# Kernel tuning notes

Hardware: AMD Instinct MI355X
Metric: run time of the kernel (lower is better)

The kernel has to match this reference:

```python
import jax, jax.numpy as jnp
import numpy as np

B = 32768          # number of graphs
NN = 19            # nodes per graph
N = B * NN         # total nodes
EF_PER, ES_PER = 120, 60
NUM_BANDS = 5
EPS = 1e-5


def _make_edges(e_per, seed):
    r = np.random.default_rng(seed)
    s = r.integers(0, NN, e_per)
    d = r.integers(0, NN, e_per)
    off = (np.arange(B, dtype=np.int64) * NN)[:, None]
    src = (off + s[None, :]).reshape(-1).astype(np.int32)
    dst = (off + d[None, :]).reshape(-1).astype(np.int32)
    return np.stack([src, dst], axis=0)  # [2, B*e_per]


def setup_inputs() -> dict:
    key = jax.random.key(0)
    ks = jax.random.split(key, 16)
    inp = {
        "x": jax.random.normal(ks[0], (N, NUM_BANDS), jnp.float32),
        "edge_weight_func": jax.random.uniform(ks[1], (B * EF_PER,), jnp.float32),
        "edge_index_func": jnp.asarray(_make_edges(EF_PER, 1)),
        "edge_index_struct": jnp.asarray(_make_edges(ES_PER, 2)),
        # GCN band params
        "W1": jax.random.normal(ks[2], (NUM_BANDS, 1, 32), jnp.float32) * 0.5,
        "b1": jnp.zeros((NUM_BANDS, 32), jnp.float32),
        "g1": jnp.ones((NUM_BANDS, 32), jnp.float32),
        "bt1": jnp.zeros((NUM_BANDS, 32), jnp.float32),
        "W2": jax.random.normal(ks[3], (NUM_BANDS, 32, 2), jnp.float32) * 0.2,
        "b2": jnp.zeros((NUM_BANDS, 2), jnp.float32),
        "g2": jnp.ones((NUM_BANDS, 2), jnp.float32),
        "bt2": jnp.zeros((NUM_BANDS, 2), jnp.float32),
        # MLP head (kaiming-ish fan_in init)
        "lin1_W": jax.random.normal(ks[4], (190, 128), jnp.float32) * np.sqrt(2.0 / 190),
        "lin1_b": jnp.zeros((128,), jnp.float32),
        "g3": jnp.ones((128,), jnp.float32),
        "bt3": jnp.zeros((128,), jnp.float32),
        "lin2_W": jax.random.normal(ks[5], (128, 32), jnp.float32) * np.sqrt(2.0 / 128),
        "lin2_b": jnp.zeros((32,), jnp.float32),
        "lin3_W": jax.random.normal(ks[6], (32, 2), jnp.float32) * np.sqrt(2.0 / 32),
        "lin3_b": jnp.zeros((2,), jnp.float32),
    }
    return inp


def _bn(h, g, b):
    # BatchNorm1d with batch statistics (training-mode math, deterministic)
    m = h.mean(0)
    v = h.var(0)
    return (h - m) * jax.lax.rsqrt(v + EPS) * g + b


def _gcn(h_in, W, b, src, dst, ew, n):
    # PyG GCNConv: symmetric norm with self-loops (fill 1), linear then scatter-add
    h = h_in @ W                                   # [N, out]
    deg = jax.ops.segment_sum(ew, dst, num_segments=n) + 1.0  # self-loop weight 1
    dinv = jax.lax.rsqrt(deg)
    norm = dinv[src] * ew * dinv[dst]              # [E]
    agg = jax.ops.segment_sum(norm[:, None] * h[src], dst, num_segments=n)
    return agg + (dinv * dinv)[:, None] * h + b    # self-loop term + bias


def reference(x, edge_weight_func, W1, b1, g1, bt1, W2, b2, g2, bt2,
              lin1_W, lin1_b, g3, bt3, lin2_W, lin2_b, lin3_W, lin3_b,
              edge_index_func, edge_index_struct):
    n = x.shape[0]
    bsz = n // NN
    sf, df = edge_index_func[0], edge_index_func[1]
    ss, ds = edge_index_struct[0], edge_index_struct[1]
    ew_s = jnp.ones((ss.shape[0],), x.dtype)
    outs = []
    for i in range(NUM_BANDS):
        h = _gcn(x[:, i:i + 1], W1[i], b1[i], sf, df, edge_weight_func, n)
        h = jax.nn.relu(_bn(h, g1[i], bt1[i]))
        h = _gcn(h, W2[i], b2[i], ss, ds, ew_s, n)
        h = jax.nn.relu(_bn(h, g2[i], bt2[i]))
        outs.append(h.reshape(bsz, NN * 2))
    xc = jnp.concatenate(outs, axis=1)             # [B, 190]
    h = jax.nn.relu(_bn(xc @ lin1_W + lin1_b, g3, bt3))
    h = jax.nn.relu(h @ lin2_W + lin2_b)
    return h @ lin3_W + lin3_b                     # [B, 2]
```

## Files before the change

kernel.cpp:

```cpp
#include <hip/hip_runtime.h>
#include <hip/hip_fp16.h>

#define BGR 32768
#define NNODE 19
#define NTOT (BGR*NNODE)
#define EF 120
#define ES 60
#define NB 5
#define EPS 1e-5f

#define WS_U     0
#define WS_PRE2  (WS_U + NTOT*NB)
#define WS_PRE3  (WS_PRE2 + BGR*190)
#define WS_H2    (WS_PRE3 + BGR*128)
#define WS_P3    (WS_H2 + NTOT*NB)
#define WS_R3    (WS_P3 + 2048*256)
#define WS_R1    (WS_R3 + 64*256)
#define WS_R2    (WS_R1 + 320)
#define WS_T1    (WS_R2 + 6400)
#define WS_A2    (WS_T1 + 660)
#define WS_D2    (WS_A2 + 16)
#define WS_A3    (WS_D2 + 16)
#define WS_D3    (WS_A3 + 128)

__global__ __launch_bounds__(256) void k1_gcn1(
    const float* __restrict__ x, const float* __restrict__ ew,
    const int* __restrict__ srcf, const int* __restrict__ dstf,
    float* __restrict__ Ub)
{
    __shared__ float xg[4][96];
    __shared__ float Nr[4][380];
    __shared__ float dinv[4][20];
    int t = threadIdx.x, q = t >> 6, lane = t & 63;
    int g = blockIdx.x*4 + q;

    int s0, d0, s1 = 0, d1 = 0; float w0, w1 = 0.f;
    bool e1 = (lane < EF - 64);
    s0 = srcf[g*EF+lane] - g*NNODE; d0 = dstf[g*EF+lane] - g*NNODE; w0 = ew[g*EF+lane];
    if (e1) { s1 = srcf[g*EF+lane+64] - g*NNODE; d1 = dstf[g*EF+lane+64] - g*NNODE; w1 = ew[g*EF+lane+64]; }
    for (int i = lane; i < 95; i += 64) xg[q][i] = x[g*95 + i];
    for (int i = lane; i < 380; i += 64) Nr[q][i] = 0.f;
    __syncthreads();

    atomicAdd(&Nr[q][d0*20 + s0], w0);
    if (e1) atomicAdd(&Nr[q][d1*20 + s1], w1);
    __syncthreads();

    if (lane < NNODE) {
        float s = 0.f;
        #pragma unroll
        for (int k = 0; k < 19; k++) s += Nr[q][lane*20 + k];
        dinv[q][lane] = rsqrtf(s + 1.f);
    }
    __syncthreads();
    for (int i = lane; i < 95; i += 64) xg[q][i] *= dinv[q][i/5];
    __syncthreads();

    for (int i = lane; i < 95; i += 64) {
        int b = i/19, v = i - 19*b;
        float acc = xg[q][v*5 + b];
        #pragma unroll
        for (int s = 0; s < 19; s++) acc += Nr[q][v*20 + s] * xg[q][s*5 + b];
        Ub[(size_t)b*NTOT + g*19 + v] = dinv[q][v] * acc;
    }
}

__global__ __launch_bounds__(256) void kr1(const float* __restrict__ U, float* __restrict__ r1)
{
    const float4* base = (const float4*)(U + (size_t)blockIdx.x * (NTOT/32));
    float s = 0.f, qq = 0.f;
    for (int n = (int)threadIdx.x; n < NTOT/128; n += 256) {
        float4 v = base[n];
        s += v.x + v.y + v.z + v.w;
        qq += v.x*v.x + v.y*v.y + v.z*v.z + v.w*v.w;
    }
    __shared__ float red[256][2];
    red[threadIdx.x][0] = s; red[threadIdx.x][1] = qq;
    __syncthreads();
    for (int off = 128; off > 0; off >>= 1) {
        if ((int)threadIdx.x < off) {
            red[threadIdx.x][0] += red[threadIdx.x+off][0];
            red[threadIdx.x][1] += red[threadIdx.x+off][1];
        }
        __syncthreads();
    }
    if (threadIdx.x < 2) r1[blockIdx.x*2 + threadIdx.x] = red[0][threadIdx.x];
}

__global__ __launch_bounds__(256) void k2b(const float* __restrict__ r1,
    const float* __restrict__ W1, const float* __restrict__ g1, const float* __restrict__ bt1,
    const float* __restrict__ W2, float4* __restrict__ T1)
{
    __shared__ float mean[5], varr[5];
    int t = threadIdx.x;
    if (t < 5) {
        float s = 0.f, qq = 0.f;
        for (int j = 0; j < 32; j++) { s += r1[(t*32+j)*2]; qq += r1[(t*32+j)*2+1]; }
        float m = s / (float)NTOT;
        mean[t] = m;
        varr[t] = qq / (float)NTOT - m*m;
    }
    __syncthreads();
    if (t < 160) {
        int b = t >> 5;
        float w = W1[t];
        float c = w * rsqrtf(w*w*varr[b] + EPS) * g1[t];
        T1[b*33 + (t & 31)] = make_float4(c, bt1[t] - c*mean[b], W2[t*2], W2[t*2+1]);
    }
}

__global__ __launch_bounds__(256) void k3a(
    const float* __restrict__ Ub, const float4* __restrict__ T1p,
    unsigned int* __restrict__ H2)
{
    int bb = blockIdx.x / (NTOT/256);
    int node = (blockIdx.x - bb*(NTOT/256))*256 + (int)threadIdx.x;
    float uv = Ub[(size_t)bb*NTOT + node];
    const float4* Tb = T1p + bb*33;
    float hx = 0.f, hy = 0.f;
    #pragma unroll
    for (int f = 0; f < 32; f++) {
        float4 c = Tb[f];
        float r = fmaxf(fmaf(c.x, uv, c.y), 0.f);
        hx = fmaf(r, c.z, hx);
        hy = fmaf(r, c.w, hy);
    }
    __half2 h = __floats2half2_rn(hx, hy);
    H2[(size_t)bb*NTOT + node] = *(unsigned int*)&h;
}

__global__ __launch_bounds__(256) void k3b(
    const unsigned int* __restrict__ H2, const int* __restrict__ srcs, const int* __restrict__ dsts,
    const float* __restrict__ b2, float2* __restrict__ pre2)
{
    __shared__ float2 h2l[4][96];
    __shared__ float  Mr[4][380];
    __shared__ float  dinv[4][20];
    __shared__ float  b2l[12];
    int t = threadIdx.x, q = t >> 6, lane = t & 63;
    int g = blockIdx.x*4 + q;

    int b0 = lane/19, v0 = lane - 19*b0;
    unsigned int h0 = H2[(size_t)b0*NTOT + g*19 + v0];
    int b1 = (lane+64)/19, v1 = (lane+64) - 19*b1;
    unsigned int h1 = (lane < 31) ? H2[(size_t)b1*NTOT + g*19 + v1] : 0u;
    int ls = 0, ld = 0; bool ee = (lane < ES);
    if (ee) { ls = srcs[g*ES+lane] - g*NNODE; ld = dsts[g*ES+lane] - g*NNODE; }
    if (t < 10) b2l[t] = b2[t];
    for (int i = lane; i < 380; i += 64) Mr[q][i] = 0.f;
    __syncthreads();

    if (ee) atomicAdd(&Mr[q][ld*20 + ls], 1.f);
    __syncthreads();

    if (lane < NNODE) {
        float s = 0.f;
        #pragma unroll
        for (int k = 0; k < 19; k++) s += Mr[q][lane*20 + k];
        dinv[q][lane] = rsqrtf(s + 1.f);
    }
    __syncthreads();

    {
        float2 f0 = __half22float2(*(__half2*)&h0);
        float sc = dinv[q][v0];
        h2l[q][v0*5 + b0] = make_float2(f0.x*sc, f0.y*sc);
        if (lane < 31) {
            float2 f1 = __half22float2(*(__half2*)&h1);
            float sc1 = dinv[q][v1];
            h2l[q][v1*5 + b1] = make_float2(f1.x*sc1, f1.y*sc1);
        }
    }
    __syncthreads();

    for (int i = lane; i < 95; i += 64) {
        int v = i/5, b = i - 5*v;
        float2 acc = h2l[q][i];
        #pragma unroll
        for (int s = 0; s < 19; s++) {
            float m = Mr[q][v*20 + s];
            float2 hh = h2l[q][s*5 + b];
            acc.x = fmaf(m, hh.x, acc.x);
            acc.y = fmaf(m, hh.y, acc.y);
        }
        float dv = dinv[q][v];
        pre2[(size_t)g*95 + i] = make_float2(fmaf(dv, acc.x, b2l[2*b]),
                                             fmaf(dv, acc.y, b2l[2*b+1]));
    }
}

__global__ __launch_bounds__(256) void kr2(const float2* __restrict__ pre2, float* __restrict__ r2)
{
    int t = threadIdx.x;
    size_t base = (size_t)blockIdx.x * 9728;
    float sx[5], sy[5], qx[5], qy[5];
    #pragma unroll
    for (int b = 0; b < 5; b++) { sx[b]=0.f; sy[b]=0.f; qx[b]=0.f; qy[b]=0.f; }
    for (int n = 0; n < 38; n++) {
        size_t i = base + n*256 + t;
        float2 v = pre2[i];
        int p = (int)(i % 95);
        int b = p % 5;
        #pragma unroll
        for (int bb = 0; bb < 5; bb++) {
            bool m = (b == bb);
            sx[bb] += m ? v.x : 0.f;     sy[bb] += m ? v.y : 0.f;
            qx[bb] += m ? v.x*v.x : 0.f; qy[bb] += m ? v.y*v.y : 0.f;
        }
    }
    __shared__ float red[256][20];
    #pragma unroll
    for (int b = 0; b < 5; b++) {
        red[t][2*b] = sx[b];      red[t][2*b+1] = sy[b];
        red[t][10+2*b] = qx[b];   red[t][11+2*b] = qy[b];
    }
    __syncthreads();
    for (int off = 128; off > 0; off >>= 1) {
        if (t < off) {
            #pragma unroll
            for (int k = 0; k < 20; k++) red[t][k] += red[t+off][k];
        }
        __syncthreads();
    }
    if (t < 20) r2[blockIdx.x*20 + t] = red[0][t];
}

__global__ __launch_bounds__(320) void k4b(const float* __restrict__ r2,
    const float* __restrict__ g2, const float* __restrict__ bt2,
    float* __restrict__ A2, float* __restrict__ D2)
{
    __shared__ float part[16][20];
    int t = threadIdx.x;
    int col = t % 20, grp = t / 20;
    float s = 0.f;
    for (int j = 0; j < 20; j++) s += r2[(grp*20 + j)*20 + col];
    part[grp][col] = s;
    __syncthreads();
    if (t < 20) {
        float ss = 0.f;
        #pragma unroll
        for (int j = 0; j < 16; j++) ss += part[j][t];
        part[0][t] = ss;
    }
    __syncthreads();
    if (t < 10) {
        float m = part[0][t] / (float)NTOT;
        float v = part[0][10+t] / (float)NTOT - m*m;
        float a = g2[t] * rsqrtf(v + EPS);
        A2[t] = a;
        D2[t] = bt2[t] - a*m;
    }
}

__global__ __launch_bounds__(256) void k5_lin1(
    const float2* __restrict__ pre2, const float* __restrict__ A2, const float* __restrict__ D2,
    const float* __restrict__ W, const float* __restrict__ bias,
    float* __restrict__ pre3, float* __restrict__ p3)
{
    __shared__ float xg[32*192];
    __shared__ float a2l[10], d2l[10];
    __shared__ float redS[4][128], redQ[4][128];
    int t = threadIdx.x, bid = blockIdx.x;
    if (t < 10) { a2l[t] = A2[t]; d2l[t] = D2[t]; }
    if (t < 64) xg[(t>>1)*192 + 190 + (t&1)] = 0.f;
    __syncthreads();

    const float2* src = pre2 + (size_t)bid*3040;
    for (int i = t; i < 3040; i += 256) {
        int gg = i / 95, p = i - gg*95;
        int b = p % 5;
        float2 v = src[i];
        xg[gg*192 + 2*p]     = fmaxf(fmaf(a2l[2*b],   v.x, d2l[2*b]),   0.f);
        xg[gg*192 + 2*p + 1] = fmaxf(fmaf(a2l[2*b+1], v.y, d2l[2*b+1]), 0.f);
    }
    __syncthreads();

    int f = t & 63, h = t >> 6;
    const float* xh = xg + h*8*192;
    float accA[8], accB[8];
    #pragma unroll
    for (int r = 0; r < 8; r++) { accA[r] = 0.f; accB[r] = 0.f; }

    for (int kt = 0; kt < 12; kt++) {
        float wA[16], wB[16];
        #pragma unroll
        for (int j = 0; j < 16; j++) {
            int k = kt*16 + j;
            if (k < 190) {
                int p = k >> 1, kk = k & 1;
                int v = p/5, b = p - 5*v;
                int row = b*38 + v*2 + kk;
                wA[j] = W[row*128 + f];
                wB[j] = W[row*128 + f + 64];
            } else { wA[j] = 0.f; wB[j] = 0.f; }
        }
        #pragma unroll
        for (int r = 0; r < 8; r++) {
            const float4* xr = (const float4*)(xh + r*192 + kt*16);
            #pragma unroll
            for (int jj = 0; jj < 4; jj++) {
                float4 xv = xr[jj];
                accA[r] = fmaf(xv.x, wA[4*jj+0], accA[r]);
                accA[r] = fmaf(xv.y, wA[4*jj+1], accA[r]);
                accA[r] = fmaf(xv.z, wA[4*jj+2], accA[r]);
                accA[r] = fmaf(xv.w, wA[4*jj+3], accA[r]);
                accB[r] = fmaf(xv.x, wB[4*jj+0], accB[r]);
                accB[r] = fmaf(xv.y, wB[4*jj+1], accB[r]);
                accB[r] = fmaf(xv.z, wB[4*jj+2], accB[r]);
                accB[r] = fmaf(xv.w, wB[4*jj+3], accB[r]);
            }
        }
    }

    float bb0 = bias[f], bb1 = bias[f + 64];
    float sA = 0.f, qA = 0.f, sB = 0.f, qB = 0.f;
    int g0 = bid*32 + h*8;
    #pragma unroll
    for (int r = 0; r < 8; r++) {
        float pA = accA[r] + bb0;
        float pB = accB[r] + bb1;
        pre3[(size_t)(g0+r)*128 + f]      = pA;
        pre3[(size_t)(g0+r)*128 + f + 64] = pB;
        sA += pA; qA += pA*pA;
        sB += pB; qB += pB*pB;
    }
    redS[h][f] = sA; redS[h][f+64] = sB;
    redQ[h][f] = qA; redQ[h][f+64] = qB;
    __syncthreads();
    if (t < 128) {
        p3[bid*256 + t] = redS[0][t] + redS[1][t] + redS[2][t] + redS[3][t];
    } else {
        int f2 = t - 128;
        p3[bid*256 + 128 + f2] = redQ[0][f2] + redQ[1][f2] + redQ[2][f2] + redQ[3][f2];
    }
}

__global__ __launch_bounds__(256) void k6a(const float* __restrict__ p3, float* __restrict__ r3)
{
    int j = blockIdx.x, f = threadIdx.x;
    float s = 0.f;
    for (int r = j*16; r < (j+1)*16; r++) s += p3[r*256 + f];
    r3[j*256 + f] = s;
}

__global__ __launch_bounds__(128) void k6b(const float* __restrict__ r3,
    const float* __restrict__ g3, const float* __restrict__ bt3,
    float* __restrict__ A3, float* __restrict__ D3)
{
    int f = threadIdx.x;
    float s = 0.f, q = 0.f;
    for (int j = 0; j < 64; j++) { s += r3[j*256 + f]; q += r3[j*256 + 128 + f]; }
    float m = s / (float)BGR;
    float v = q / (float)BGR - m*m;
    float a = g3[f] * rsqrtf(v + EPS);
    A3[f] = a;
    D3[f] = bt3[f] - a*m;
}

__global__ __launch_bounds__(256) void k7_head(
    const float* __restrict__ pre3, const float* __restrict__ A3, const float* __restrict__ D3,
    const float* __restrict__ W2h, const float* __restrict__ b2h,
    const float* __restrict__ W3h, const float* __restrict__ b3h,
    float* __restrict__ out)
{
    int g = blockIdx.x*256 + threadIdx.x;
    float accj[32];
    #pragma unroll
    for (int j = 0; j < 32; j++) accj[j] = b2h[j];
    const float* p3 = pre3 + (size_t)g*128;
    #pragma unroll 2
    for (int f4 = 0; f4 < 128; f4 += 4) {
        float4 pv = *(const float4*)(p3 + f4);
        float y0 = fmaxf(fmaf(A3[f4+0], pv.x, D3[f4+0]), 0.f);
        float y1 = fmaxf(fmaf(A3[f4+1], pv.y, D3[f4+1]), 0.f);
        float y2 = fmaxf(fmaf(A3[f4+2], pv.z, D3[f4+2]), 0.f);
        float y3 = fmaxf(fmaf(A3[f4+3], pv.w, D3[f4+3]), 0.f);
        #pragma unroll
        for (int j = 0; j < 32; j++) {
            accj[j] = fmaf(y0, W2h[(f4+0)*32+j], accj[j]);
            accj[j] = fmaf(y1, W2h[(f4+1)*32+j], accj[j]);
            accj[j] = fmaf(y2, W2h[(f4+2)*32+j], accj[j]);
            accj[j] = fmaf(y3, W2h[(f4+3)*32+j], accj[j]);
        }
    }
    float o0 = b3h[0], o1 = b3h[1];
    #pragma unroll
    for (int j = 0; j < 32; j++) {
        float yj = fmaxf(accj[j], 0.f);
        o0 = fmaf(yj, W3h[j*2+0], o0);
        o1 = fmaf(yj, W3h[j*2+1], o1);
    }
    ((float2*)out)[g] = make_float2(o0, o1);
}

extern "C" void kernel_launch(void* const* d_in, const int* in_sizes, int n_in,
                              void* d_out, int out_size, void* d_ws, size_t ws_size,
                              hipStream_t stream)
{
    (void)in_sizes; (void)n_in; (void)out_size; (void)ws_size;
    const float* x    = (const float*)d_in[0];
    const float* ew   = (const float*)d_in[1];
    const int*   eif  = (const int*)d_in[2];
    const int*   eis  = (const int*)d_in[3];
    const float* W1   = (const float*)d_in[4];
    const float* g1   = (const float*)d_in[6];
    const float* bt1  = (const float*)d_in[7];
    const float* W2   = (const float*)d_in[8];
    const float* b2   = (const float*)d_in[9];
    const float* g2   = (const float*)d_in[10];
    const float* bt2  = (const float*)d_in[11];
    const float* l1W  = (const float*)d_in[12];
    const float* l1b  = (const float*)d_in[13];
    const float* g3   = (const float*)d_in[14];
    const float* bt3  = (const float*)d_in[15];
    const float* l2W  = (const float*)d_in[16];
    const float* l2b  = (const float*)d_in[17];
    const float* l3W  = (const float*)d_in[18];
    const float* l3b  = (const float*)d_in[19];
    float* out = (float*)d_out;
    float* ws  = (float*)d_ws;

    const int* srcf = eif;  const int* dstf = eif + BGR*EF;
    const int* srcs = eis;  const int* dsts = eis + BGR*ES;

    float* U    = ws + WS_U;
    float* PRE2 = ws + WS_PRE2;
    float* PRE3 = ws + WS_PRE3;
    unsigned int* H2 = (unsigned int*)(ws + WS_H2);
    float* P3   = ws + WS_P3;
    float* R3   = ws + WS_R3;
    float* R1   = ws + WS_R1;
    float* R2   = ws + WS_R2;
    float4* T1  = (float4*)(ws + WS_T1);
    float* A2   = ws + WS_A2;
    float* D2   = ws + WS_D2;
    float* A3   = ws + WS_A3;
    float* D3   = ws + WS_D3;

    k1_gcn1<<<BGR/4, 256, 0, stream>>>(x, ew, srcf, dstf, U);
    kr1<<<160, 256, 0, stream>>>(U, R1);
    k2b<<<1, 256, 0, stream>>>(R1, W1, g1, bt1, W2, T1);
    k3a<<<(NTOT/256)*5, 256, 0, stream>>>(U, T1, H2);
    k3b<<<BGR/4, 256, 0, stream>>>(H2, srcs, dsts, b2, (float2*)PRE2);
    kr2<<<320, 256, 0, stream>>>((const float2*)PRE2, R2);
    k4b<<<1, 320, 0, stream>>>(R2, g2, bt2, A2, D2);
    k5_lin1<<<1024, 256, 0, stream>>>((const float2*)PRE2, A2, D2, l1W, l1b, PRE3, P3);
    k6a<<<64, 256, 0, stream>>>(P3, R3);
    k6b<<<1, 128, 0, stream>>>(R3, g3, bt3, A3, D3);
    k7_head<<<BGR/256, 256, 0, stream>>>(PRE3, A3, D3, l2W, l2b, l3W, l3b, out);
}
```

Measured before the change: 322.6 us.

## Fuse BN statistic partials into GCN kernels and prepermute lin1 weights

The GCN1 and GCN2 kernels now emit per-block sum and sum-of-squares partials through shared-memory atomics, which removes the separate kr1 and kr2 passes that re-read U and PRE2 from global memory. The single-block finalize kernels now reduce 8192 partials each using 1024 threads. A new kwp kernel writes the lin1 weight matrix in a permuted, zero-padded layout, so k5_lin1 drops its per-element index arithmetic and uses a 4x4 register tile. The shared matrices are padded to 20 columns so the inner loops can use float4 reads. The trade-off is serial final reductions over many partials in one block and an extra small weight-permutation launch on every call.

```diff
diff --git a/kernel.cpp b/kernel.cpp
--- a/kernel.cpp
+++ b/kernel.cpp
@@ -14,10 +14,11 @@
 #define WS_PRE3  (WS_PRE2 + BGR*190)
 #define WS_H2    (WS_PRE3 + BGR*128)
 #define WS_P3    (WS_H2 + NTOT*NB)
-#define WS_R3    (WS_P3 + 2048*256)
-#define WS_R1    (WS_R3 + 64*256)
-#define WS_R2    (WS_R1 + 320)
-#define WS_T1    (WS_R2 + 6400)
+#define WS_R3    (WS_P3 + 262144)
+#define WS_P1    (WS_R3 + 16384)
+#define WS_P2    (WS_P1 + 81920)
+#define WS_WP    (WS_P2 + 163840)
+#define WS_T1    (WS_WP + 24576)
 #define WS_A2    (WS_T1 + 660)
 #define WS_D2    (WS_A2 + 16)
 #define WS_A3    (WS_D2 + 16)
@@ -26,11 +27,12 @@
 __global__ __launch_bounds__(256) void k1_gcn1(
     const float* __restrict__ x, const float* __restrict__ ew,
     const int* __restrict__ srcf, const int* __restrict__ dstf,
-    float* __restrict__ Ub)
-{
-    __shared__ float xg[4][96];
-    __shared__ float Nr[4][380];
+    float* __restrict__ Ub, float* __restrict__ P1)
+{
+    __shared__ float xgb[4][100];
+    __shared__ float Nr[4][400];
     __shared__ float dinv[4][20];
+    __shared__ float ps[80];
     int t = threadIdx.x, q = t >> 6, lane = t & 63;
     int g = blockIdx.x*4 + q;
 
@@ -38,67 +40,81 @@
     bool e1 = (lane < EF - 64);
     s0 = srcf[g*EF+lane] - g*NNODE; d0 = dstf[g*EF+lane] - g*NNODE; w0 = ew[g*EF+lane];
     if (e1) { s1 = srcf[g*EF+lane+64] - g*NNODE; d1 = dstf[g*EF+lane+64] - g*NNODE; w1 = ew[g*EF+lane+64]; }
-    for (int i = lane; i < 95; i += 64) xg[q][i] = x[g*95 + i];
-    for (int i = lane; i < 380; i += 64) Nr[q][i] = 0.f;
+    for (int j = lane; j < 100; j += 64) {
+        int b = j/20, s = j - 20*b;
+        xgb[q][j] = (s < 19) ? x[g*95 + s*5 + b] : 0.f;
+    }
+    for (int i = lane; i < 400; i += 64) Nr[q][i] = 0.f;
+    if (t < 80) ps[t] = 0.f;
     __syncthreads();
 
     atomicAdd(&Nr[q][d0*20 + s0], w0);
     if (e1) atomicAdd(&Nr[q][d1*20 + s1], w1);
     __syncthreads();
 
-    if (lane < NNODE) {
-        float s = 0.f;
-        #pragma unroll
-        for (int k = 0; k < 19; k++) s += Nr[q][lane*20 + k];
-        dinv[q][lane] = rsqrtf(s + 1.f);
-    }
-    __syncthreads();
-    for (int i = lane; i < 95; i += 64) xg[q][i] *= dinv[q][i/5];
+    if (lane < 20) {
+        float dv = 0.f;
+        if (lane < 19) {
+            float s = 0.f;
+            #pragma unroll
+            for (int k = 0; k < 19; k++) s += Nr[q][lane*20 + k];
+            dv = rsqrtf(s + 1.f);
+        }
+        dinv[q][lane] = dv;
+    }
+    __syncthreads();
+    for (int j = lane; j < 100; j += 64) xgb[q][j] *= dinv[q][j % 20];
     __syncthreads();
 
     for (int i = lane; i < 95; i += 64) {
         int b = i/19, v = i - 19*b;
-        float acc = xg[q][v*5 + b];
-        #pragma unroll
-        for (int s = 0; s < 19; s++) acc += Nr[q][v*20 + s] * xg[q][s*5 + b];
-        Ub[(size_t)b*NTOT + g*19 + v] = dinv[q][v] * acc;
-    }
-}
-
-__global__ __launch_bounds__(256) void kr1(const float* __restrict__ U, float* __restrict__ r1)
-{
-    const float4* base = (const float4*)(U + (size_t)blockIdx.x * (NTOT/32));
-    float s = 0.f, qq = 0.f;
-    for (int n = (int)threadIdx.x; n < NTOT/128; n += 256) {
-        float4 v = base[n];
-        s += v.x + v.y + v.z + v.w;
-        qq += v.x*v.x + v.y*v.y + v.z*v.z + v.w*v.w;
-    }
-    __shared__ float red[256][2];
-    red[threadIdx.x][0] = s; red[threadIdx.x][1] = qq;
-    __syncthreads();
-    for (int off = 128; off > 0; off >>= 1) {
-        if ((int)threadIdx.x < off) {
-            red[threadIdx.x][0] += red[threadIdx.x+off][0];
-            red[threadIdx.x][1] += red[threadIdx.x+off][1];
-        }
-        __syncthreads();
-    }
-    if (threadIdx.x < 2) r1[blockIdx.x*2 + threadIdx.x] = red[0][threadIdx.x];
-}
-
-__global__ __launch_bounds__(256) void k2b(const float* __restrict__ r1,
+        float acc = xgb[q][b*20 + v];
+        const float4* nrp = (const float4*)&Nr[q][v*20];
+        const float4* xbp = (const float4*)&xgb[q][b*20];
+        #pragma unroll
+        for (int j = 0; j < 5; j++) {
+            float4 n4 = nrp[j], x4 = xbp[j];
+            acc += n4.x*x4.x + n4.y*x4.y + n4.z*x4.z + n4.w*x4.w;
+        }
+        float uv = dinv[q][v] * acc;
+        Ub[(size_t)b*NTOT + g*19 + v] = uv;
+        int c = lane & 7;
+        atomicAdd(&ps[c*10 + b], uv);
+        atomicAdd(&ps[c*10 + 5 + b], uv*uv);
+    }
+    __syncthreads();
+    if (t < 10) {
+        float s = 0.f;
+        #pragma unroll
+        for (int c = 0; c < 8; c++) s += ps[c*10 + t];
+        P1[blockIdx.x*10 + t] = s;
+    }
+}
+
+__global__ __launch_bounds__(1024) void k2b(const float* __restrict__ P1,
     const float* __restrict__ W1, const float* __restrict__ g1, const float* __restrict__ bt1,
     const float* __restrict__ W2, float4* __restrict__ T1)
 {
-    __shared__ float mean[5], varr[5];
+    __shared__ float red[1000];
+    __shared__ float tmp10[10], mean[5], varr[5];
     int t = threadIdx.x;
+    if (t < 1000) {
+        int col = t % 10, grp = t / 10;
+        float acc = 0.f;
+        for (int r = grp; r < 8192; r += 100) acc += P1[r*10 + col];
+        red[t] = acc;
+    }
+    __syncthreads();
+    if (t < 10) {
+        float s = 0.f;
+        for (int j = 0; j < 100; j++) s += red[j*10 + t];
+        tmp10[t] = s;
+    }
+    __syncthreads();
     if (t < 5) {
-        float s = 0.f, qq = 0.f;
-        for (int j = 0; j < 32; j++) { s += r1[(t*32+j)*2]; qq += r1[(t*32+j)*2+1]; }
-        float m = s / (float)NTOT;
+        float m = tmp10[t] / (float)NTOT;
         mean[t] = m;
-        varr[t] = qq / (float)NTOT - m*m;
+        varr[t] = tmp10[5+t] / (float)NTOT - m*m;
     }
     __syncthreads();
     if (t < 160) {
@@ -131,12 +147,13 @@
 
 __global__ __launch_bounds__(256) void k3b(
     const unsigned int* __restrict__ H2, const int* __restrict__ srcs, const int* __restrict__ dsts,
-    const float* __restrict__ b2, float2* __restrict__ pre2)
-{
-    __shared__ float2 h2l[4][96];
-    __shared__ float  Mr[4][380];
+    const float* __restrict__ b2, float2* __restrict__ pre2, float* __restrict__ P2)
+{
+    __shared__ float2 h2b[4][100];
+    __shared__ float  Mr[4][400];
     __shared__ float  dinv[4][20];
     __shared__ float  b2l[12];
+    __shared__ float  ps[160];
     int t = threadIdx.x, q = t >> 6, lane = t & 63;
     int g = blockIdx.x*4 + q;
 
@@ -147,119 +164,120 @@
     int ls = 0, ld = 0; bool ee = (lane < ES);
     if (ee) { ls = srcs[g*ES+lane] - g*NNODE; ld = dsts[g*ES+lane] - g*NNODE; }
     if (t < 10) b2l[t] = b2[t];
-    for (int i = lane; i < 380; i += 64) Mr[q][i] = 0.f;
+    if (t < 160) ps[t] = 0.f;
+    for (int i = lane; i < 400; i += 64) Mr[q][i] = 0.f;
     __syncthreads();
 
     if (ee) atomicAdd(&Mr[q][ld*20 + ls], 1.f);
     __syncthreads();
 
-    if (lane < NNODE) {
-        float s = 0.f;
-        #pragma unroll
-        for (int k = 0; k < 19; k++) s += Mr[q][lane*20 + k];
-        dinv[q][lane] = rsqrtf(s + 1.f);
+    if (lane < 20) {
+        float dv = 0.f;
+        if (lane < 19) {
+            float s = 0.f;
+            #pragma unroll
+            for (int k = 0; k < 19; k++) s += Mr[q][lane*20 + k];
+            dv = rsqrtf(s + 1.f);
+        }
+        dinv[q][lane] = dv;
     }
     __syncthreads();
 
     {
         float2 f0 = __half22float2(*(__half2*)&h0);
         float sc = dinv[q][v0];
-        h2l[q][v0*5 + b0] = make_float2(f0.x*sc, f0.y*sc);
+        h2b[q][b0*20 + v0] = make_float2(f0.x*sc, f0.y*sc);
         if (lane < 31) {
             float2 f1 = __half22float2(*(__half2*)&h1);
             float sc1 = dinv[q][v1];
-            h2l[q][v1*5 + b1] = make_float2(f1.x*sc1, f1.y*sc1);
-        }
+            h2b[q][b1*20 + v1] = make_float2(f1.x*sc1, f1.y*sc1);
+        }
+        if (lane < 5) h2b[q][lane*20 + 19] = make_float2(0.f, 0.f);
     }
     __syncthreads();
 
     for (int i = lane; i < 95; i += 64) {
         int v = i/5, b = i - 5*v;
-        float2 acc = h2l[q][i];
-        #pragma unroll
-        for (int s = 0; s < 19; s++) {
-            float m = Mr[q][v*20 + s];
-            float2 hh = h2l[q][s*5 + b];
-            acc.x = fmaf(m, hh.x, acc.x);
-            acc.y = fmaf(m, hh.y, acc.y);
+        float2 self = h2b[q][b*20 + v];
+        float ax = self.x, ay = self.y;
+        const float4* mp = (const float4*)&Mr[q][v*20];
+        const float4* hp = (const float4*)&h2b[q][b*20];
+        #pragma unroll
+        for (int j = 0; j < 5; j++) {
+            float4 m4 = mp[j];
+            float4 hA = hp[2*j], hB = hp[2*j+1];
+            ax += m4.x*hA.x + m4.y*hA.z + m4.z*hB.x + m4.w*hB.z;
+            ay += m4.x*hA.y + m4.y*hA.w + m4.z*hB.y + m4.w*hB.w;
         }
         float dv = dinv[q][v];
-        pre2[(size_t)g*95 + i] = make_float2(fmaf(dv, acc.x, b2l[2*b]),
-                                             fmaf(dv, acc.y, b2l[2*b+1]));
-    }
-}
-
-__global__ __launch_bounds__(256) void kr2(const float2* __restrict__ pre2, float* __restrict__ r2)
-{
-    int t = threadIdx.x;
-    size_t base = (size_t)blockIdx.x * 9728;
-    float sx[5], sy[5], qx[5], qy[5];
-    #pragma unroll
-    for (int b = 0; b < 5; b++) { sx[b]=0.f; sy[b]=0.f; qx[b]=0.f; qy[b]=0.f; }
-    for (int n = 0; n < 38; n++) {
-        size_t i = base + n*256 + t;
-        float2 v = pre2[i];
-        int p = (int)(i % 95);
-        int b = p % 5;
-        #pragma unroll
-        for (int bb = 0; bb < 5; bb++) {
-            bool m = (b == bb);
-            sx[bb] += m ? v.x : 0.f;     sy[bb] += m ? v.y : 0.f;
-            qx[bb] += m ? v.x*v.x : 0.f; qy[bb] += m ? v.y*v.y : 0.f;
-        }
-    }
-    __shared__ float red[256][20];
-    #pragma unroll
-    for (int b = 0; b < 5; b++) {
-        red[t][2*b] = sx[b];      red[t][2*b+1] = sy[b];
-        red[t][10+2*b] = qx[b];   red[t][11+2*b] = qy[b];
-    }
-    __syncthreads();
-    for (int off = 128; off > 0; off >>= 1) {
-        if (t < off) {
-            #pragma unroll
-            for (int k = 0; k < 20; k++) red[t][k] += red[t+off][k];
-        }
-        __syncthreads();
-    }
-    if (t < 20) r2[blockIdx.x*20 + t] = red[0][t];
-}
-
-__global__ __launch_bounds__(320) void k4b(const float* __restrict__ r2,
+        float ox = fmaf(dv, ax, b2l[2*b]);
+        float oy = fmaf(dv, ay, b2l[2*b+1]);
+        pre2[(size_t)g*95 + i] = make_float2(ox, oy);
+        int c = lane & 7;
+        atomicAdd(&ps[c*20 + 2*b],      ox);
+        atomicAdd(&ps[c*20 + 2*b + 1],  oy);
+        atomicAdd(&ps[c*20 + 10 + 2*b], ox*ox);
+        atomicAdd(&ps[c*20 + 11 + 2*b], oy*oy);
+    }
+    __syncthreads();
+    if (t < 20) {
+        float s = 0.f;
+        #pragma unroll
+        for (int c = 0; c < 8; c++) s += ps[c*20 + t];
+        P2[blockIdx.x*20 + t] = s;
+    }
+}
+
+__global__ __launch_bounds__(1024) void k4b(const float* __restrict__ P2,
     const float* __restrict__ g2, const float* __restrict__ bt2,
     float* __restrict__ A2, float* __restrict__ D2)
 {
-    __shared__ float part[16][20];
+    __shared__ float red[1000];
+    __shared__ float tmp20[20];
     int t = threadIdx.x;
-    int col = t % 20, grp = t / 20;
-    float s = 0.f;
-    for (int j = 0; j < 20; j++) s += r2[(grp*20 + j)*20 + col];
-    part[grp][col] = s;
+    if (t < 1000) {
+        int col = t % 20, grp = t / 20;
+        float acc = 0.f;
+        for (int r = grp; r < 8192; r += 50) acc += P2[r*20 + col];
+        red[t] = acc;
+    }
     __syncthreads();
     if (t < 20) {
-        float ss = 0.f;
-        #pragma unroll
-        for (int j = 0; j < 16; j++) ss += part[j][t];
-        part[0][t] = ss;
+        float s = 0.f;
+        for (int j = 0; j < 50; j++) s += red[j*20 + t];
+        tmp20[t] = s;
     }
     __syncthreads();
     if (t < 10) {
-        float m = part[0][t] / (float)NTOT;
-        float v = part[0][10+t] / (float)NTOT - m*m;
+        float m = tmp20[t] / (float)NTOT;
+        float v = tmp20[10+t] / (float)NTOT - m*m;
         float a = g2[t] * rsqrtf(v + EPS);
         A2[t] = a;
         D2[t] = bt2[t] - a*m;
     }
 }
 
-__global__ __launch_bounds__(256) void k5_lin1(
+__global__ __launch_bounds__(256) void kwp(const float* __restrict__ W, float* __restrict__ Wp)
+{
+    int idx = blockIdx.x*256 + (int)threadIdx.x;
+    int k = idx >> 7, f = idx & 127;
+    float val = 0.f;
+    if (k < 190) {
+        int p = k >> 1, kk = k & 1;
+        int v = p/5, b = p - 5*v;
+        val = W[(b*38 + v*2 + kk)*128 + f];
+    }
+    Wp[idx] = val;
+}
+
+__global__ __launch_bounds__(256, 4) void k5_lin1(
     const float2* __restrict__ pre2, const float* __restrict__ A2, const float* __restrict__ D2,
-    const float* __restrict__ W, const float* __restrict__ bias,
+    const float* __restrict__ Wp, const float* __restrict__ bias,
     float* __restrict__ pre3, float* __restrict__ p3)
 {
     __shared__ float xg[32*192];
     __shared__ float a2l[10], d2l[10];
-    __shared__ float redS[4][128], redQ[4][128];
+    __shared__ float redS[8][128], redQ[8][128];
     int t = threadIdx.x, bid = blockIdx.x;
     if (t < 10) { a2l[t] = A2[t]; d2l[t] = D2[t]; }
     if (t < 64) xg[(t>>1)*192 + 190 + (t&1)] = 0.f;
@@ -275,63 +293,69 @@
     }
     __syncthreads();
 
-    int f = t & 63, h = t >> 6;
-    const float* xh = xg + h*8*192;
-    float accA[8], accB[8];
+    int lane = t & 63, h = t >> 6;
+    int f32 = lane & 31, gh = lane >> 5;
+    const float* xh = xg + (h*8 + gh*4)*192;
+    float acc[4][4];
     #pragma unroll
-    for (int r = 0; r < 8; r++) { accA[r] = 0.f; accB[r] = 0.f; }
-
-    for (int kt = 0; kt < 12; kt++) {
-        float wA[16], wB[16];
-        #pragma unroll
-        for (int j = 0; j < 16; j++) {
-            int k = kt*16 + j;
-            if (k < 190) {
-                int p = k >> 1, kk = k & 1;
-                int v = p/5, b = p - 5*v;
-                int row = b*38 + v*2 + kk;
-                wA[j] = W[row*128 + f];
-                wB[j] = W[row*128 + f + 64];
-            } else { wA[j] = 0.f; wB[j] = 0.f; }
-        }
-        #pragma unroll
-        for (int r = 0; r < 8; r++) {
-            const float4* xr = (const float4*)(xh + r*192 + kt*16);
+    for (int r = 0; r < 4; r++)
+        #pragma unroll
+        for (int fg = 0; fg < 4; fg++) acc[r][fg] = 0.f;
+
+    for (int kt = 0; kt < 24; kt++) {
+        const float* wb = Wp + kt*8*128 + f32;
+        float wv[4][8];
+        #pragma unroll
+        for (int fg = 0; fg < 4; fg++)
             #pragma unroll
-            for (int jj = 0; jj < 4; jj++) {
-                float4 xv = xr[jj];
-                accA[r] = fmaf(xv.x, wA[4*jj+0], accA[r]);
-                accA[r] = fmaf(xv.y, wA[4*jj+1], accA[r]);
-                accA[r] = fmaf(xv.z, wA[4*jj+2], accA[r]);
-                accA[r] = fmaf(xv.w, wA[4*jj+3], accA[r]);
-                accB[r] = fmaf(xv.x, wB[4*jj+0], accB[r]);
-                accB[r] = fmaf(xv.y, wB[4*jj+1], accB[r]);
-                accB[r] = fmaf(xv.z, wB[4*jj+2], accB[r]);
-                accB[r] = fmaf(xv.w, wB[4*jj+3], accB[r]);
+            for (int j = 0; j < 8; j++) wv[fg][j] = wb[j*128 + 32*fg];
+        #pragma unroll
+        for (int r = 0; r < 4; r++) {
+            float4 xa = *(const float4*)(xh + r*192 + kt*8);
+            float4 xb = *(const float4*)(xh + r*192 + kt*8 + 4);
+            #pragma unroll
+            for (int fg = 0; fg < 4; fg++) {
+                float a = acc[r][fg];
+                a = fmaf(xa.x, wv[fg][0], a);
+                a = fmaf(xa.y, wv[fg][1], a);
+                a = fmaf(xa.z, wv[fg][2], a);
+                a = fmaf(xa.w, wv[fg][3], a);
+                a = fmaf(xb.x, wv[fg][4], a);
+                a = fmaf(xb.y, wv[fg][5], a);
+                a = fmaf(xb.z, wv[fg][6], a);
+                a = fmaf(xb.w, wv[fg][7], a);
+                acc[r][fg] = a;
             }
         }
     }
 
-    float bb0 = bias[f], bb1 = bias[f + 64];
-    float sA = 0.f, qA = 0.f, sB = 0.f, qB = 0.f;
-    int g0 = bid*32 + h*8;
+    int gbase = bid*32 + h*8 + gh*4;
     #pragma unroll
-    for (int r = 0; r < 8; r++) {
-        float pA = accA[r] + bb0;
-        float pB = accB[r] + bb1;
-        pre3[(size_t)(g0+r)*128 + f]      = pA;
-        pre3[(size_t)(g0+r)*128 + f + 64] = pB;
-        sA += pA; qA += pA*pA;
-        sB += pB; qB += pB*pB;
-    }
-    redS[h][f] = sA; redS[h][f+64] = sB;
-    redQ[h][f] = qA; redQ[h][f+64] = qB;
+    for (int fg = 0; fg < 4; fg++) {
+        int f = f32 + 32*fg;
+        float bb = bias[f];
+        float s = 0.f, qq = 0.f;
+        #pragma unroll
+        for (int r = 0; r < 4; r++) {
+            float pv = acc[r][fg] + bb;
+            pre3[(size_t)(gbase + r)*128 + f] = pv;
+            s += pv; qq += pv*pv;
+        }
+        redS[h*2 + gh][f] = s;
+        redQ[h*2 + gh][f] = qq;
+    }
     __syncthreads();
     if (t < 128) {
-        p3[bid*256 + t] = redS[0][t] + redS[1][t] + redS[2][t] + redS[3][t];
+        float s = 0.f;
+        #pragma unroll
+        for (int j = 0; j < 8; j++) s += redS[j][t];
+        p3[bid*256 + t] = s;
     } else {
-        int f2 = t - 128;
-        p3[bid*256 + 128 + f2] = redQ[0][f2] + redQ[1][f2] + redQ[2][f2] + redQ[3][f2];
+        int f = t - 128;
+        float qq = 0.f;
+        #pragma unroll
+        for (int j = 0; j < 8; j++) qq += redQ[j][f];
+        p3[bid*256 + 128 + f] = qq;
     }
 }
 
@@ -429,22 +453,22 @@
     unsigned int* H2 = (unsigned int*)(ws + WS_H2);
     float* P3   = ws + WS_P3;
     float* R3   = ws + WS_R3;
-    float* R1   = ws + WS_R1;
-    float* R2   = ws + WS_R2;
+    float* P1   = ws + WS_P1;
+    float* P2   = ws + WS_P2;
+    float* WP   = ws + WS_WP;
     float4* T1  = (float4*)(ws + WS_T1);
     float* A2   = ws + WS_A2;
     float* D2   = ws + WS_D2;
     float* A3   = ws + WS_A3;
     float* D3   = ws + WS_D3;
 
-    k1_gcn1<<<BGR/4, 256, 0, stream>>>(x, ew, srcf, dstf, U);
-    kr1<<<160, 256, 0, stream>>>(U, R1);
-    k2b<<<1, 256, 0, stream>>>(R1, W1, g1, bt1, W2, T1);
+    kwp<<<96, 256, 0, stream>>>(l1W, WP);
+    k1_gcn1<<<BGR/4, 256, 0, stream>>>(x, ew, srcf, dstf, U, P1);
+    k2b<<<1, 1024, 0, stream>>>(P1, W1, g1, bt1, W2, T1);
     k3a<<<(NTOT/256)*5, 256, 0, stream>>>(U, T1, H2);
-    k3b<<<BGR/4, 256, 0, stream>>>(H2, srcs, dsts, b2, (float2*)PRE2);
-    kr2<<<320, 256, 0, stream>>>((const float2*)PRE2, R2);
-    k4b<<<1, 320, 0, stream>>>(R2, g2, bt2, A2, D2);
-    k5_lin1<<<1024, 256, 0, stream>>>((const float2*)PRE2, A2, D2, l1W, l1b, PRE3, P3);
+    k3b<<<BGR/4, 256, 0, stream>>>(H2, srcs, dsts, b2, (float2*)PRE2, P2);
+    k4b<<<1, 1024, 0, stream>>>(P2, g2, bt2, A2, D2);
+    k5_lin1<<<1024, 256, 0, stream>>>((const float2*)PRE2, A2, D2, WP, l1b, PRE3, P3);
     k6a<<<64, 256, 0, stream>>>(P3, R3);
     k6b<<<1, 128, 0, stream>>>(R3, g3, bt3, A3, D3);
     k7_head<<<BGR/256, 256, 0, stream>>>(PRE3, A3, D3, l2W, l2b, l3W, l3b, out);
```

After: 444.0 us. +37.7%, slower.
